# Performance work log

Hardware: AMD Instinct MI355X
Metric: run time of the kernel (lower is better)

## Reference

```python
import jax, jax.numpy as jnp
import numpy as np

N_TOKENS = 32768
DIM = 2048
N_EXPERTS = 256
N_GROUPS = 8
N_LIMITED_GROUPS = 4
TOP_K = 8
ROUTE_SCALE = 2.5


def setup_inputs() -> dict:
    key = jax.random.key(0)
    k1, k2, k3, k4 = jax.random.split(key, 4)
    x = jax.random.normal(k1, (N_TOKENS, DIM), dtype=jnp.float32)
    w1 = jax.random.normal(k2, (N_EXPERTS, DIM), dtype=jnp.float32) * (DIM ** -0.5)
    b_lin = jax.random.normal(k3, (N_EXPERTS,), dtype=jnp.float32) * 0.02
    bias = jax.random.normal(k4, (N_EXPERTS,), dtype=jnp.float32) * 0.02
    return {"x": x, "w1": w1, "b_lin": b_lin, "bias": bias}


def reference(x, w1, b_lin, bias):
    n = x.shape[0]
    # gate GEMM: [N, dim] x [dim, E] -> [N, E]
    logits = jnp.einsum("nd,ed->ne", x, w1) + b_lin
    # sigmoid scoring with L1 normalization
    s = jax.nn.sigmoid(logits)
    s = s / jnp.sum(s, axis=-1, keepdims=True)
    # routing-correction bias (torch code adds it in place, so it is also in the
    # gathered values via the original_scores alias)
    s = s + bias
    original_scores = s
    # group-limited masking: keep only top n_limited_groups groups (amax score,
    # since use_bias=True)
    g = s.reshape(n, N_GROUPS, N_EXPERTS // N_GROUPS)
    group_scores = jnp.max(g, axis=-1)                      # [N, G]
    _, gidx = jax.lax.top_k(group_scores, N_LIMITED_GROUPS)  # [N, Glim]
    keep = jnp.zeros((n, N_GROUPS), dtype=bool).at[
        jnp.arange(n)[:, None], gidx].set(True)
    masked = jnp.where(keep[:, :, None], g, -jnp.inf).reshape(n, N_EXPERTS)
    # final top-k over masked scores, gather from (bias-added) original scores
    _, indices = jax.lax.top_k(masked, TOP_K)               # [N, k]
    values = jnp.take_along_axis(original_scores, indices, axis=1) * ROUTE_SCALE
    return values.astype(x.dtype), indices
```

## Files before the change

### kernel.cpp

```cpp
#include <hip/hip_runtime.h>
#include <math.h>

#define NTOK   32768
#define DIM    2048
#define NE     256
#define NG     8
#define GSZ    32
#define NLIM   4
#define TOPK   8
#define RSCALE 2.5f
#define TAU    4e-7f

#define BT      64
#define THREADS 256
#define KT      16
#define NKT     (DIM / KT)
#define WOFF    262144
#define TILE_B  16384

typedef __bf16 bf16x8 __attribute__((ext_vector_type(8)));
typedef float  f32x16 __attribute__((ext_vector_type(16)));

typedef const __attribute__((address_space(1))) void GASV;
typedef __attribute__((address_space(3))) void LASV;

__device__ __forceinline__ void gload16(const void* g, void* l) {
    __builtin_amdgcn_global_load_lds((GASV*)g, (LASV*)l, 16, 0, 0);
}

__device__ __forceinline__ void split_pack(float4 a, float4 b,
                                           bf16x8& h8, bf16x8& r8) {
    float v[8] = {a.x, a.y, a.z, a.w, b.x, b.y, b.z, b.w};
    union { unsigned int u[4]; bf16x8 v8; } H, R;
#pragma unroll
    for (int q = 0; q < 4; ++q) {
        const unsigned int u0 = __float_as_uint(v[2 * q]);
        const unsigned int u1 = __float_as_uint(v[2 * q + 1]);
        H.u[q] = (u0 >> 16) | (u1 & 0xFFFF0000u);
        const float r0 = v[2 * q]     - __uint_as_float(u0 & 0xFFFF0000u);
        const float r1 = v[2 * q + 1] - __uint_as_float(u1 & 0xFFFF0000u);
        R.u[q] = (__float_as_uint(r0) >> 16) |
                 (__float_as_uint(r1) & 0xFFFF0000u);
    }
    h8 = H.v8; r8 = R.v8;
}

__global__ __launch_bounds__(256) void wsplit_kernel(
    const float* __restrict__ w1, unsigned int* __restrict__ wt)
{
    const int g  = blockIdx.x * 256 + threadIdx.x;
    const int e  = g & 255;
    const int hi = (g >> 8) & 1;
    const int p  = (g >> 9) & 1;
    const int kt = g >> 10;
    const float* src = w1 + (size_t)e * DIM + kt * 16 + hi * 8;

    uint4 o;
    unsigned int w[4];
#pragma unroll
    for (int q = 0; q < 4; ++q) {
        const float v0 = src[2 * q], v1 = src[2 * q + 1];
        const unsigned int u0 = __float_as_uint(v0);
        const unsigned int u1 = __float_as_uint(v1);
        if (p == 0) {
            w[q] = (u0 >> 16) | (u1 & 0xFFFF0000u);
        } else {
            const float r0 = v0 - __uint_as_float(u0 & 0xFFFF0000u);
            const float r1 = v1 - __uint_as_float(u1 & 0xFFFF0000u);
            w[q] = (__float_as_uint(r0) >> 16) |
                   (__float_as_uint(r1) & 0xFFFF0000u);
        }
    }
    o.x = w[0]; o.y = w[1]; o.z = w[2]; o.w = w[3];
    *(uint4*)(wt + (size_t)g * 4) = o;
}

__global__ __launch_bounds__(THREADS, 3) void router_pass1(
    const float* __restrict__ x, const unsigned int* __restrict__ wt,
    const float* __restrict__ b_lin, const float* __restrict__ bias,
    float* __restrict__ out_vals, float* __restrict__ out_idx,
    int* __restrict__ wsI)
{
    __shared__ union {
        char  B[3 * TILE_B];
        float sc[32 * 260];
    } sm;

    const int tid  = threadIdx.x;
    const int lane = tid & 63;
    const int wave = tid >> 6;
    const int l31  = lane & 31;
    const int hi   = lane >> 5;
    const int wm   = wave >> 1;
    const int wn   = wave & 1;
    const int t0   = blockIdx.x * BT;

    const float4* xrow =
        (const float4*)(x + (size_t)(t0 + wm * 32 + l31) * DIM) + hi * 2;

    const char* wsrc = (const char*)wt;

    char* p_cur = sm.B;
    char* p_nxt = sm.B + TILE_B;
    char* p_stg = sm.B + 2 * TILE_B;

    auto STAGE = [&](char* ldsbase, int kt) {
#pragma unroll
        for (int q = 0; q < 4; ++q) {
            const int chunk = wave * 4 + q;
            gload16(wsrc + (size_t)kt * TILE_B + chunk * 1024 + lane * 16,
                    ldsbase + chunk * 1024);
        }
    };

    f32x16 acc[4] = {};

    STAGE(p_cur, 0);
    STAGE(p_nxt, 1);
    asm volatile("" ::: "memory");
    float4 f0 = xrow[0];
    float4 f1 = xrow[1];

    const int e_base = (wn * 128 + l31) * 16;
    const int hi4k   = hi * 4096;

    for (int kt = 0; kt < NKT; ++kt) {
        if (kt + 1 < NKT) asm volatile("s_waitcnt vmcnt(6)" ::: "memory");
        else              asm volatile("s_waitcnt vmcnt(2)" ::: "memory");
        asm volatile("s_barrier" ::: "memory");

        float4 nf0, nf1;
        if (kt + 1 < NKT) {
            nf0 = xrow[(kt + 1) * 4];
            nf1 = xrow[(kt + 1) * 4 + 1];
        }

        bf16x8 ah, ar;
        split_pack(f0, f1, ah, ar);

#pragma unroll
        for (int j = 0; j < 4; ++j) {
            const int eo = e_base + j * 512;
            bf16x8 bh = *(const bf16x8*)(p_cur + hi4k + eo);
            bf16x8 br = *(const bf16x8*)(p_cur + 8192 + hi4k + eo);
            acc[j] = __builtin_amdgcn_mfma_f32_32x32x16_bf16(ah, bh, acc[j], 0, 0, 0);
            acc[j] = __builtin_amdgcn_mfma_f32_32x32x16_bf16(ah, br, acc[j], 0, 0, 0);
            acc[j] = __builtin_amdgcn_mfma_f32_32x32x16_bf16(ar, bh, acc[j], 0, 0, 0);
        }

        if (kt + 2 < NKT) STAGE(p_stg, kt + 2);

        f0 = nf0; f1 = nf1;
        char* t = p_cur; p_cur = p_nxt; p_nxt = p_stg; p_stg = t;
    }

    __syncthreads();

    const int tx = tid & 31;
    const int ty = tid >> 5;
    float blv[8], bsv[8];
#pragma unroll
    for (int j = 0; j < 8; ++j) {
        blv[j] = b_lin[tx + 32 * j];
        bsv[j] = bias[tx + 32 * j];
    }

    for (int h = 0; h < 2; ++h) {
        if (h) __syncthreads();
        if (wm == h) {
#pragma unroll
            for (int j = 0; j < 4; ++j) {
#pragma unroll
                for (int r = 0; r < 16; ++r) {
                    const int row = (r & 3) + 8 * (r >> 2) + 4 * hi;
                    const int e   = wn * 128 + j * 32 + l31;
                    sm.sc[row * 260 + e] = acc[j][r];
                }
            }
        }
        __syncthreads();

#pragma unroll
        for (int i = 0; i < 4; ++i) {
            const int row = ty * 4 + i;
            float s8[8];
            float psum = 0.0f;
#pragma unroll
            for (int j = 0; j < 8; ++j) {
                const float lg = sm.sc[row * 260 + tx + 32 * j] + blv[j];
                const float s = 1.0f / (1.0f + expf(-lg));
                s8[j] = s;
                psum += s;
            }
#pragma unroll
            for (int m = 1; m <= 16; m <<= 1) psum += __shfl_xor(psum, m);
#pragma unroll
            for (int j = 0; j < 8; ++j) s8[j] = s8[j] / psum + bsv[j];

            float gm[8];
#pragma unroll
            for (int j = 0; j < 8; ++j) gm[j] = s8[j];
#pragma unroll
            for (int m = 1; m <= 16; m <<= 1)
#pragma unroll
                for (int j = 0; j < 8; ++j)
                    gm[j] = fmaxf(gm[j], __shfl_xor(gm[j], m));

            unsigned keep = 0u;
            float g4v = 0.0f, g5v = 0.0f;
#pragma unroll
            for (int r = 0; r < 5; ++r) {
                float bv = -1e30f; int bg = 0;
#pragma unroll
                for (int g = 0; g < 8; ++g)
                    if (!((keep >> g) & 1) && gm[g] > bv) { bv = gm[g]; bg = g; }
                if (r < 4) { keep |= 1u << bg; g4v = bv; }
                else g5v = bv;
            }
            float margin = g4v - g5v;

#pragma unroll
            for (int j = 0; j < 8; ++j)
                if (!((keep >> j) & 1)) s8[j] = -1e30f;

            float tv[9]; int te[9];
#pragma unroll
            for (int r = 0; r < 9; ++r) {
                float bv = -1e30f; int bj = 8;
#pragma unroll
                for (int j = 0; j < 8; ++j)
                    if (s8[j] > bv) { bv = s8[j]; bj = j; }
                int be = (bj < 8) ? (tx + 32 * bj) : 9999;
#pragma unroll
                for (int m = 1; m <= 16; m <<= 1) {
                    const float ov = __shfl_xor(bv, m);
                    const int   oe = __shfl_xor(be, m);
                    if (ov > bv || (ov == bv && oe < be)) { bv = ov; be = oe; }
                }
                tv[r] = bv; te[r] = be;
                if (r < 8 && (be & 31) == tx) s8[be >> 5] = -1e30f;
            }
#pragma unroll
            for (int r = 0; r < 8; ++r) margin = fminf(margin, tv[r] - tv[r + 1]);

            if (tx == 0) {
                const int t = t0 + h * 32 + row;
                const int base = t * TOPK;
#pragma unroll
                for (int r = 0; r < 8; ++r) {
                    out_vals[base + r] = tv[r] * RSCALE;
                    out_idx[base + r]  = (float)te[r];
                }
                if (margin < TAU) {
                    const int slot = atomicAdd(&wsI[0], 1);
                    if (slot < 60000) wsI[4 + slot] = t;
                }
            }
        }
    }
}

__global__ __launch_bounds__(THREADS, 1) void router_pass2(
    const float* __restrict__ x, const float* __restrict__ w1,
    const float* __restrict__ b_lin, const float* __restrict__ bias,
    float* __restrict__ out_vals, float* __restrict__ out_idx,
    const int* __restrict__ wsI)
{
    __shared__ double xrow[DIM];
    __shared__ double red[256];
    __shared__ double sc[NE];

    const int tid = threadIdx.x;
    const int count = min(wsI[0], 60000);
    const int* list = wsI + 4;
    const float4* x4 = (const float4*)x;
    const float4* w4 = (const float4*)w1;

    for (int li = blockIdx.x; li < count; li += gridDim.x) {
        const int t = list[li];
        __syncthreads();
#pragma unroll
        for (int q = 0; q < 2; ++q) {
            const int id = tid + 256 * q;
            const float4 v = x4[t * 512 + id];
            xrow[id * 4 + 0] = (double)v.x;
            xrow[id * 4 + 1] = (double)v.y;
            xrow[id * 4 + 2] = (double)v.z;
            xrow[id * 4 + 3] = (double)v.w;
        }
        __syncthreads();

        const int e = tid;
        double a0 = 0.0, a1 = 0.0, a2 = 0.0, a3 = 0.0;
#pragma unroll 2
        for (int k4 = 0; k4 < 512; k4 += 4) {
#pragma unroll
            for (int z = 0; z < 4; ++z) {
                const float4 wv = w4[e * 512 + k4 + z];
                double* ac = (z == 0) ? &a0 : (z == 1) ? &a1 : (z == 2) ? &a2 : &a3;
                *ac = fma(xrow[(k4 + z) * 4 + 0], (double)wv.x, *ac);
                *ac = fma(xrow[(k4 + z) * 4 + 1], (double)wv.y, *ac);
                *ac = fma(xrow[(k4 + z) * 4 + 2], (double)wv.z, *ac);
                *ac = fma(xrow[(k4 + z) * 4 + 3], (double)wv.w, *ac);
            }
        }
        const double lg = ((a0 + a1) + (a2 + a3)) + (double)b_lin[e];
        const double s = 1.0 / (1.0 + exp(-lg));
        red[tid] = s;
        __syncthreads();
        for (int off = 128; off > 0; off >>= 1) {
            if (tid < off) red[tid] += red[tid + off];
            __syncthreads();
        }
        sc[e] = s / red[0] + (double)bias[e];
        __syncthreads();

        if (tid == 0) {
            double gmax[NG];
            for (int g = 0; g < NG; ++g) {
                double mx = -INFINITY;
                for (int q = 0; q < GSZ; ++q) {
                    const double v = sc[g * GSZ + q];
                    mx = (v > mx) ? v : mx;
                }
                gmax[g] = mx;
            }
            unsigned keep = 0u;
            for (int r = 0; r < NLIM; ++r) {
                int best = 0; double bv = -INFINITY;
                for (int g = 0; g < NG; ++g) {
                    if (keep & (1u << g)) continue;
                    if (gmax[g] > bv) { bv = gmax[g]; best = g; }
                }
                keep |= 1u << best;
            }
            double tv[TOPK]; int ti[TOPK];
            for (int r = 0; r < TOPK; ++r) { tv[r] = -INFINITY; ti[r] = NE; }
            for (int g = 0; g < NG; ++g) {
                if (!(keep & (1u << g))) continue;
                for (int q = 0; q < GSZ; ++q) {
                    const int ee = g * GSZ + q;
                    const double v = sc[ee];
                    if (v > tv[TOPK - 1]) {
                        int p = TOPK - 1;
                        while (p > 0 && v > tv[p - 1]) {
                            tv[p] = tv[p - 1]; ti[p] = ti[p - 1]; --p;
                        }
                        tv[p] = v; ti[p] = ee;
                    }
                }
            }
            const int base = t * TOPK;
            for (int r = 0; r < TOPK; ++r) {
                out_vals[base + r] = (float)(tv[r] * (double)RSCALE);
                out_idx[base + r]  = (float)ti[r];
            }
        }
    }
}

extern "C" void kernel_launch(void* const* d_in, const int* in_sizes, int n_in,
                              void* d_out, int out_size, void* d_ws, size_t ws_size,
                              hipStream_t stream) {
    const float* x     = (const float*)d_in[0];
    const float* w1    = (const float*)d_in[1];
    const float* b_lin = (const float*)d_in[2];
    const float* bias  = (const float*)d_in[3];
    float* out_vals = (float*)d_out;
    float* out_idx  = (float*)d_out + (size_t)NTOK * TOPK;

    int* wsI = (int*)d_ws;
    unsigned int* wt = (unsigned int*)((char*)d_ws + WOFF);

    hipMemsetAsync(d_ws, 0, 16, stream);
    wsplit_kernel<<<dim3(512), 256, 0, stream>>>(w1, wt);
    router_pass1<<<dim3(NTOK / BT), THREADS, 0, stream>>>(
        x, wt, b_lin, bias, out_vals, out_idx, wsI);
    router_pass2<<<dim3(256), THREADS, 0, stream>>>(
        x, w1, b_lin, bias, out_vals, out_idx, (const int*)d_ws);
}
```

Baseline: 271.0 us.

## Deepen x-row register prefetch and issue weight staging before MFMAs

The x-row register prefetch in the gate GEMM main loop now runs two K-tiles ahead instead of one. The async LDS staging of the weight tile for kt+2 is now issued right after the barrier, before the MFMA block, rather than after it. Scheduling barriers pin this memory-issue order, and s_setprio raises wave priority around the MFMAs to favour compute overlap. The goal is to hide global-load latency on the large x stream, at the cost of extra VGPRs for the deeper x buffers, which may affect occupancy at 3 blocks per SIMD.

```diff
diff --git a/kernel.cpp b/kernel.cpp
--- a/kernel.cpp
+++ b/kernel.cpp
@@ -82,7 +82,7 @@
     int* __restrict__ wsI)
 {
     __shared__ union {
-        char  B[3 * TILE_B];
+        alignas(16) char B[3 * TILE_B];
         float sc[32 * 260];
     } sm;
 
@@ -115,29 +115,38 @@
 
     f32x16 acc[4] = {};
 
+    float4 xa0 = xrow[0], xa1 = xrow[1];
+    __builtin_amdgcn_sched_barrier(0);
     STAGE(p_cur, 0);
+    __builtin_amdgcn_sched_barrier(0);
+    float4 xb0 = xrow[4], xb1 = xrow[5];
+    __builtin_amdgcn_sched_barrier(0);
     STAGE(p_nxt, 1);
-    asm volatile("" ::: "memory");
-    float4 f0 = xrow[0];
-    float4 f1 = xrow[1];
+    __builtin_amdgcn_sched_barrier(0);
 
     const int e_base = (wn * 128 + l31) * 16;
     const int hi4k   = hi * 4096;
 
     for (int kt = 0; kt < NKT; ++kt) {
-        if (kt + 1 < NKT) asm volatile("s_waitcnt vmcnt(6)" ::: "memory");
-        else              asm volatile("s_waitcnt vmcnt(2)" ::: "memory");
-        asm volatile("s_barrier" ::: "memory");
-
-        float4 nf0, nf1;
-        if (kt + 1 < NKT) {
-            nf0 = xrow[(kt + 1) * 4];
-            nf1 = xrow[(kt + 1) * 4 + 1];
+        if (kt < NKT - 1) asm volatile("s_waitcnt vmcnt(6)");
+        else              asm volatile("s_waitcnt vmcnt(0)");
+        __builtin_amdgcn_sched_barrier(0);
+        __builtin_amdgcn_s_barrier();
+        __builtin_amdgcn_sched_barrier(0);
+
+        float4 xc0, xc1;
+        if (kt + 2 < NKT) {
+            xc0 = xrow[(kt + 2) * 4];
+            xc1 = xrow[(kt + 2) * 4 + 1];
+            __builtin_amdgcn_sched_barrier(0);
+            STAGE(p_stg, kt + 2);
+            __builtin_amdgcn_sched_barrier(0);
         }
 
         bf16x8 ah, ar;
-        split_pack(f0, f1, ah, ar);
-
+        split_pack(xa0, xa1, ah, ar);
+
+        __builtin_amdgcn_s_setprio(1);
 #pragma unroll
         for (int j = 0; j < 4; ++j) {
             const int eo = e_base + j * 512;
@@ -147,10 +156,9 @@
             acc[j] = __builtin_amdgcn_mfma_f32_32x32x16_bf16(ah, br, acc[j], 0, 0, 0);
             acc[j] = __builtin_amdgcn_mfma_f32_32x32x16_bf16(ar, bh, acc[j], 0, 0, 0);
         }
-
-        if (kt + 2 < NKT) STAGE(p_stg, kt + 2);
-
-        f0 = nf0; f1 = nf1;
+        __builtin_amdgcn_s_setprio(0);
+
+        xa0 = xb0; xa1 = xb1; xb0 = xc0; xb1 = xc1;
         char* t = p_cur; p_cur = p_nxt; p_nxt = p_stg; p_stg = t;
     }
 
```

After: 268.4 us. About the same (-0.9%).
